# Kernel tuning notes

Hardware: AMD Instinct MI355X
Metric: run time of the kernel (lower is better)

The kernel has to match this reference:

```python
import jax, jax.numpy as jnp
import numpy as np

B = 64        # graphs per batch
NPG = 512     # nodes per graph (batch = repeat(arange(B), NPG))
D = 128       # hidden_dim = input_dim
L = 3         # GCN layers
K = 16        # NTN tensors
BINS = 16     # histogram bins


def _prep_edges(ei, N, dtype):
    # GCNConv normalization: add self-loops, deg on targets, sym norm
    loop = jnp.arange(N)
    src = jnp.concatenate([ei[0], loop])
    dst = jnp.concatenate([ei[1], loop])
    deg = jnp.zeros((N,), dtype).at[dst].add(1.0)
    dinv = jnp.where(deg > 0, jax.lax.rsqrt(deg), 0.0)
    norm = (dinv[src] * dinv[dst])[:, None]
    return src, dst, norm


def _encode(x, src, dst, norm, gcn_w, gcn_b, bn_g, bn_b, bn_m, bn_v):
    # eval-mode BatchNorm (running stats), dropout = identity
    for l in range(L):
        h = x @ gcn_w[l].T                     # [N, D]
        x = jnp.zeros_like(h).at[dst].add(norm * h[src]) + gcn_b[l]
        x = (x - bn_m[l]) * jax.lax.rsqrt(bn_v[l] + 1e-5) * bn_g[l] + bn_b[l]
        x = jax.nn.relu(x)
    return x


def _attention_pool(emb, ctx_w, ctx_b, att_w, att_b):
    t = jnp.tanh(emb @ ctx_w.T + ctx_b)        # [N, D]
    s = (t @ att_w + att_b).reshape(B, NPG, 1)
    e = emb.reshape(B, NPG, D)
    w = jax.nn.softmax(s, axis=1)              # per-graph softmax
    return (w * e).sum(axis=1)                 # [B, D]


def _histogram(e1, e2):
    n1 = (e1 / jnp.maximum(jnp.linalg.norm(e1, axis=-1, keepdims=True), 1e-8)).reshape(B, NPG, D)
    n2 = (e2 / jnp.maximum(jnp.linalg.norm(e2, axis=-1, keepdims=True), 1e-8)).reshape(B, NPG, D)
    sims = jnp.einsum('bnd,bmd->bnm', n1, n2)  # [B, n, n] cosine sims in [-1,1]
    bi = jnp.clip(jnp.floor((sims + 1.0) * (BINS / 2.0)), 0, BINS - 1).astype(jnp.int32)
    flat = (jnp.arange(B, dtype=jnp.int32)[:, None] * BINS + bi.reshape(B, -1)).reshape(-1)
    hist = jax.ops.segment_sum(jnp.ones(flat.shape, jnp.float32), flat,
                               num_segments=B * BINS).reshape(B, BINS)
    return hist / (hist.sum(axis=1, keepdims=True) + 1e-8)


def _ntn(g1, g2, T, tb, w1, b1, w2, b2, w3, b3):
    tp = jnp.einsum('bd,kde,be->bk', g1, T, g2) + tb   # bilinear products
    h = jax.nn.relu(tp @ w1.T + b1)
    h = jax.nn.relu(h @ w2.T + b2)
    return jax.nn.sigmoid(h @ w3.T + b3)               # [B, 1]


def _forward(x1, x2, edge_index1, edge_index2,
             gcn_w, gcn_b, bn_gamma, bn_beta, bn_mean, bn_var,
             ctx_w, ctx_b, att_w, att_b,
             ntn_T, ntn_bias, ntn_w1, ntn_b1, ntn_w2, ntn_b2, ntn_w3, ntn_b3,
             hist_w1, hist_b1, hist_w2, hist_b2,
             fus_w1, fus_b1, fus_w2, fus_b2):
    N = x1.shape[0]
    s1, d1, n1 = _prep_edges(edge_index1, N, x1.dtype)
    s2, d2, n2 = _prep_edges(edge_index2, N, x2.dtype)
    e1 = _encode(x1, s1, d1, n1, gcn_w, gcn_b, bn_gamma, bn_beta, bn_mean, bn_var)
    e2 = _encode(x2, s2, d2, n2, gcn_w, gcn_b, bn_gamma, bn_beta, bn_mean, bn_var)
    g1 = _attention_pool(e1, ctx_w, ctx_b, att_w, att_b)
    g2 = _attention_pool(e2, ctx_w, ctx_b, att_w, att_b)
    ntn_sim = _ntn(g1, g2, ntn_T, ntn_bias, ntn_w1, ntn_b1, ntn_w2, ntn_b2, ntn_w3, ntn_b3)
    hist = _histogram(e1, e2)
    hemb = jax.nn.relu(hist @ hist_w1.T + hist_b1) @ hist_w2.T + hist_b2
    comb = jnp.concatenate([ntn_sim, hemb], axis=1)    # [B, 17]
    h = jax.nn.relu(comb @ fus_w1.T + fus_b1)
    return jax.nn.sigmoid(h @ fus_w2.T + fus_b2)       # [B, 1]


def setup_inputs() -> dict:
    key = jax.random.key(0)
    ks = jax.random.split(key, 32)
    N = B * NPG
    E = 16 * N
    sc = 0.05
    inp = {
        'x1': jax.random.normal(ks[0], (N, D), jnp.float32),
        'x2': jax.random.normal(ks[1], (N, D), jnp.float32),
        'edge_index1': jax.random.randint(ks[2], (2, E), 0, N),
        'edge_index2': jax.random.randint(ks[3], (2, E), 0, N),
        'batch1': jnp.repeat(jnp.arange(B), NPG),
        'batch2': jnp.repeat(jnp.arange(B), NPG),
        'gcn_w': jax.random.normal(ks[4], (L, D, D), jnp.float32) * sc,
        'gcn_b': jax.random.normal(ks[5], (L, D), jnp.float32) * sc,
        'bn_gamma': jnp.ones((L, D), jnp.float32),
        'bn_beta': jnp.zeros((L, D), jnp.float32),
        'bn_mean': jnp.zeros((L, D), jnp.float32),
        'bn_var': jnp.ones((L, D), jnp.float32),
        'ctx_w': jax.random.normal(ks[6], (D, D), jnp.float32) * sc,
        'ctx_b': jax.random.normal(ks[7], (D,), jnp.float32) * sc,
        'att_w': jax.random.normal(ks[8], (D,), jnp.float32) * sc,
        'att_b': jax.random.normal(ks[9], (1,), jnp.float32) * sc,
        'ntn_T': jax.random.normal(ks[10], (K, D, D), jnp.float32) * 0.02,
        'ntn_bias': jax.random.normal(ks[11], (K,), jnp.float32) * sc,
        'ntn_w1': jax.random.normal(ks[12], (32, K), jnp.float32) * 0.2,
        'ntn_b1': jax.random.normal(ks[13], (32,), jnp.float32) * sc,
        'ntn_w2': jax.random.normal(ks[14], (16, 32), jnp.float32) * 0.15,
        'ntn_b2': jax.random.normal(ks[15], (16,), jnp.float32) * sc,
        'ntn_w3': jax.random.normal(ks[16], (1, 16), jnp.float32) * 0.2,
        'ntn_b3': jax.random.normal(ks[17], (1,), jnp.float32) * sc,
        'hist_w1': jax.random.normal(ks[18], (32, BINS), jnp.float32) * 0.2,
        'hist_b1': jax.random.normal(ks[19], (32,), jnp.float32) * sc,
        'hist_w2': jax.random.normal(ks[20], (16, 32), jnp.float32) * 0.15,
        'hist_b2': jax.random.normal(ks[21], (16,), jnp.float32) * sc,
        'fus_w1': jax.random.normal(ks[22], (8, 17), jnp.float32) * 0.2,
        'fus_b1': jax.random.normal(ks[23], (8,), jnp.float32) * sc,
        'fus_w2': jax.random.normal(ks[24], (1, 8), jnp.float32) * 0.3,
        'fus_b2': jax.random.normal(ks[25], (1,), jnp.float32) * sc,
    }
    return inp


def reference(x1, x2, edge_index1, edge_index2, batch1, batch2,
              gcn_w, gcn_b, bn_gamma, bn_beta, bn_mean, bn_var,
              ctx_w, ctx_b, att_w, att_b,
              ntn_T, ntn_bias, ntn_w1, ntn_b1, ntn_w2, ntn_b2, ntn_w3, ntn_b3,
              hist_w1, hist_b1, hist_w2, hist_b2,
              fus_w1, fus_b1, fus_w2, fus_b2):
    # batch1/batch2 encode 64 equal-sized graphs (repeat(arange(B), NPG));
    # the per-graph loops of the torch code become dense [B, NPG, D] ops.
    return _forward(x1, x2, edge_index1, edge_index2,
                    gcn_w, gcn_b, bn_gamma, bn_beta, bn_mean, bn_var,
                    ctx_w, ctx_b, att_w, att_b,
                    ntn_T, ntn_bias, ntn_w1, ntn_b1, ntn_w2, ntn_b2, ntn_w3, ntn_b3,
                    hist_w1, hist_b1, hist_w2, hist_b2,
                    fus_w1, fus_b1, fus_w2, fus_b2)
```

## Files before the change

kernel.cpp:

```cpp
#include <hip/hip_runtime.h>
#include <math.h>

#define NN 32768
#define BB 64
#define NPG 512
#define DD 128
#define LL 3
#define EE 524288
#define NBINS 16
#define KNTN 16
#define NND (NN*DD)
#define NBKT 128
#define BSEG 56
#define BCAPE 10240

typedef unsigned short ushort_t;
typedef __attribute__((ext_vector_type(8))) short short8;
typedef __attribute__((ext_vector_type(4))) float f32x4;

__device__ __forceinline__ ushort_t f2bf(float f) {
    unsigned u = __builtin_bit_cast(unsigned, f);
    u += 0x7FFFu + ((u >> 16) & 1u);
    return (ushort_t)(u >> 16);
}
__device__ __forceinline__ float bf2f(ushort_t h) {
    unsigned u = ((unsigned)h) << 16;
    return __builtin_bit_cast(float, u);
}
__device__ __forceinline__ unsigned pack2(float a, float b) {
    return (unsigned)f2bf(a) | ((unsigned)f2bf(b) << 16);
}
__device__ __forceinline__ float lo16(unsigned u) { return __builtin_bit_cast(float, u << 16); }
__device__ __forceinline__ float hi16(unsigned u) { return __builtin_bit_cast(float, u & 0xffff0000u); }

__global__ __launch_bounds__(256) void k_bucket(const int* __restrict__ ei1,
                                                const int* __restrict__ ei2,
                                                unsigned* __restrict__ ibuf,
                                                int* __restrict__ bcnt,
                                                const float* __restrict__ gw,
                                                const float* __restrict__ cw,
                                                ushort_t* __restrict__ wbf,
                                                const float* __restrict__ gcn_b,
                                                const float* __restrict__ bn_g,
                                                const float* __restrict__ bn_b,
                                                const float* __restrict__ bn_m,
                                                const float* __restrict__ bn_v,
                                                float* __restrict__ bnsc,
                                                float* __restrict__ bnsh) {
    int t = threadIdx.x;
    int blk = blockIdx.x;
    if (blk >= 512) {
        if (blk < 576) {
            int i = (blk - 512) * 256 + t;
            const float4 v = (i < 3 * DD * DD / 4) ? ((const float4*)gw)[i]
                                                   : ((const float4*)cw)[i - 3 * DD * DD / 4];
            uint2 o;
            o.x = pack2(v.x, v.y);
            o.y = pack2(v.z, v.w);
            ((uint2*)wbf)[i] = o;
        } else if (t < DD) {
            #pragma unroll
            for (int l = 0; l < LL; l++) {
                int c = l * DD + t;
                float sc = bn_g[c] * rsqrtf(bn_v[c] + 1e-5f);
                bnsc[c] = sc;
                bnsh[c] = (gcn_b[c] - bn_m[c]) * sc + bn_b[c];
            }
        }
        return;
    }
    __shared__ int cnt[NBKT];
    const int* ei = (blk < 256) ? ei1 : ei2;
    int ebase = (blk & 255) * 2048;
    int addn = (blk < 256) ? 0 : NN;
    for (int i = t; i < NBKT; i += 256) cnt[i] = 0;
    __syncthreads();
    #pragma unroll
    for (int k = 0; k < 8; k++) {
        int e = ebase + t + k * 256;
        int s = ei[e] + addn;
        int d = ei[EE + e] + addn;
        unsigned p = (unsigned)s | ((unsigned)d << 16);
        int bk = (unsigned)d >> 9;
        int rk = atomicAdd(&cnt[bk], 1);
        ibuf[(size_t)(bk * 512 + blk) * BSEG + rk] = p;
    }
    __syncthreads();
    if (t < NBKT) bcnt[t * 512 + blk] = cnt[t];
}

__global__ __launch_bounds__(256) void k_bcsr(const unsigned* __restrict__ ibuf,
                                              const int* __restrict__ bcnt,
                                              int* __restrict__ deg,
                                              float* __restrict__ dinv,
                                              int* __restrict__ rowstart,
                                              ushort_t* __restrict__ esrc) {
    __shared__ int cnt[512];
    __shared__ int ps[256];
    __shared__ int lcur[512];
    int bk = blockIdx.x, t = threadIdx.x;
    for (int i = t; i < 512; i += 256) cnt[i] = 0;
    __syncthreads();
    for (int b = t; b < 512; b += 256) {
        int n = bcnt[bk * 512 + b];
        const unsigned* seg = ibuf + (size_t)(bk * 512 + b) * BSEG;
        for (int i = 0; i < n; i++) {
            int dl = (seg[i] >> 16) & 511;
            atomicAdd(&cnt[dl], 1);
        }
    }
    __syncthreads();
    int c0 = cnt[2 * t], c1 = cnt[2 * t + 1];
    ps[t] = c0 + c1;
    __syncthreads();
    for (int o = 1; o < 256; o <<= 1) {
        int v = (t >= o) ? ps[t - o] : 0;
        __syncthreads();
        ps[t] += v;
        __syncthreads();
    }
    int excl = (t == 0) ? 0 : ps[t - 1];
    int base = bk * BCAPE;
    int g0 = bk * 512 + 2 * t, g1 = g0 + 1;
    deg[g0] = c0; deg[g1] = c1;
    dinv[g0] = rsqrtf((float)c0 + 1.0f);
    dinv[g1] = rsqrtf((float)c1 + 1.0f);
    int r0 = base + excl, r1 = base + excl + c0;
    rowstart[g0] = r0;
    rowstart[g1] = r1;
    lcur[2 * t] = r0;
    lcur[2 * t + 1] = r1;
    __syncthreads();
    for (int b = t; b < 512; b += 256) {
        int n = bcnt[bk * 512 + b];
        const unsigned* seg = ibuf + (size_t)(bk * 512 + b) * BSEG;
        for (int i = 0; i < n; i++) {
            unsigned p = seg[i];
            int dl = (p >> 16) & 511;
            int slot = atomicAdd(&lcur[dl], 1);
            esrc[slot] = (ushort_t)(p & 0xffffu);
        }
    }
}

template<int EPI, int XF>
__global__ __launch_bounds__(256) void k_mgemm(const ushort_t* __restrict__ X,
                                               const float* __restrict__ Xf1,
                                               const float* __restrict__ Xf2,
                                               const ushort_t* __restrict__ Wb,
                                               const float* __restrict__ bias,
                                               ushort_t* __restrict__ Out,
                                               const float* __restrict__ aw,
                                               const float* __restrict__ ab,
                                               float* __restrict__ Sout,
                                               const float* __restrict__ dscale) {
    __shared__ __align__(16) ushort_t wlds[128 * 128];
    int t = threadIdx.x;
    {
        int r = t >> 1, h = t & 1;
        const uint4* src = (const uint4*)(Wb + (size_t)r * DD + h * 64);
        #pragma unroll
        for (int i = 0; i < 8; i++) {
            int co = h * 128 + i * 16;
            int sw = co ^ ((r & 7) << 4);
            *(uint4*)&wlds[r * DD + (sw >> 1)] = src[i];
        }
    }
    __syncthreads();
    int w = t >> 6, l = t & 63;
    int rw = blockIdx.x * 128 + w * 32;
    int lr = l & 15, lg = l >> 4;
    f32x4 acc[2][8];
    #pragma unroll
    for (int g = 0; g < 2; g++)
        #pragma unroll
        for (int c = 0; c < 8; c++) acc[g][c] = (f32x4){0.f, 0.f, 0.f, 0.f};
    const ushort_t* xrow0 = X + (size_t)(rw + lr) * DD + lg * 8;
    const ushort_t* xrow1 = xrow0 + (size_t)16 * DD;
    const float* xf0 = nullptr;
    if (XF) {
        const float* xb = (rw < NN) ? Xf1 : (Xf2 - (size_t)NN * DD);
        xf0 = xb + (size_t)(rw + lr) * DD + lg * 8;
    }
    int swl = (lr & 7) << 4;
    for (int kt = 0; kt < 4; kt++) {
        short8 a0, a1;
        if (XF) {
            float4 va = *(const float4*)(xf0 + kt * 32);
            float4 vb = *(const float4*)(xf0 + kt * 32 + 4);
            float4 vc = *(const float4*)(xf0 + (size_t)16 * DD + kt * 32);
            float4 vd = *(const float4*)(xf0 + (size_t)16 * DD + kt * 32 + 4);
            a0[0] = (short)f2bf(va.x); a0[1] = (short)f2bf(va.y);
            a0[2] = (short)f2bf(va.z); a0[3] = (short)f2bf(va.w);
            a0[4] = (short)f2bf(vb.x); a0[5] = (short)f2bf(vb.y);
            a0[6] = (short)f2bf(vb.z); a0[7] = (short)f2bf(vb.w);
            a1[0] = (short)f2bf(vc.x); a1[1] = (short)f2bf(vc.y);
            a1[2] = (short)f2bf(vc.z); a1[3] = (short)f2bf(vc.w);
            a1[4] = (short)f2bf(vd.x); a1[5] = (short)f2bf(vd.y);
            a1[6] = (short)f2bf(vd.z); a1[7] = (short)f2bf(vd.w);
        } else {
            a0 = *(const short8*)(xrow0 + kt * 32);
            a1 = *(const short8*)(xrow1 + kt * 32);
        }
        int colsw = (kt * 64 + lg * 16) ^ swl;
        #pragma unroll
        for (int c = 0; c < 8; c++) {
            int row = c * 16 + lr;
            short8 b = *(const short8*)&wlds[row * DD + (colsw >> 1)];
            acc[0][c] = __builtin_amdgcn_mfma_f32_16x16x32_bf16(a0, b, acc[0][c], 0, 0, 0);
            acc[1][c] = __builtin_amdgcn_mfma_f32_16x16x32_bf16(a1, b, acc[1][c], 0, 0, 0);
        }
    }
    if (EPI == 0) {
        float ds[2][4];
        #pragma unroll
        for (int g = 0; g < 2; g++)
            #pragma unroll
            for (int q = 0; q < 4; q++) ds[g][q] = dscale[rw + g * 16 + lg * 4 + q];
        #pragma unroll
        for (int g = 0; g < 2; g++)
            #pragma unroll
            for (int c = 0; c < 8; c++) {
                int col = c * 16 + lr;
                #pragma unroll
                for (int q = 0; q < 4; q++)
                    Out[(size_t)(rw + g * 16 + lg * 4 + q) * DD + col] = f2bf(acc[g][c][q] * ds[g][q]);
            }
    } else {
        float rs[2][4] = {};
        #pragma unroll
        for (int c = 0; c < 8; c++) {
            int col = c * 16 + lr;
            float bv = bias[col], wv = aw[col];
            #pragma unroll
            for (int g = 0; g < 2; g++)
                #pragma unroll
                for (int q = 0; q < 4; q++)
                    rs[g][q] += tanhf(acc[g][c][q] + bv) * wv;
        }
        #pragma unroll
        for (int m = 1; m < 16; m <<= 1)
            #pragma unroll
            for (int g = 0; g < 2; g++)
                #pragma unroll
                for (int q = 0; q < 4; q++) rs[g][q] += __shfl_xor(rs[g][q], m);
        if (lr == 0) {
            float a0 = ab[0];
            #pragma unroll
            for (int g = 0; g < 2; g++)
                #pragma unroll
                for (int q = 0; q < 4; q++)
                    Sout[rw + g * 16 + lg * 4 + q] = rs[g][q] + a0;
        }
    }
}

#define GATHER(u, s) uint4 u = Hu4[(size_t)(s) * 16 + cl]
#define ACCUM(u) \
    a0 += lo16(u.x); a1 += hi16(u.x); a2 += lo16(u.y); a3 += hi16(u.y); \
    a4 += lo16(u.z); a5 += hi16(u.z); a6 += lo16(u.w); a7 += hi16(u.w)

template<int LAST>
__global__ __launch_bounds__(256) void k_agg(
    const ushort_t* __restrict__ Hs, const int* __restrict__ rowstart,
    const int* __restrict__ deg, const ushort_t* __restrict__ esrc,
    const float* __restrict__ dinv, const float* __restrict__ bnsc,
    const float* __restrict__ bnsh, ushort_t* __restrict__ A,
    ushort_t* __restrict__ Nrm) {
    __shared__ ushort_t sidx[2048];
    int nb0 = blockIdx.x * 16;
    int blockBeg = rowstart[nb0];
    int blockCnt = rowstart[nb0 + 15] + deg[nb0 + 15] - blockBeg;
    for (int i = threadIdx.x; i < blockCnt; i += 256) sidx[i] = esrc[blockBeg + i];
    __syncthreads();
    int l = threadIdx.x & 63;
    int q = l >> 4, cl = l & 15;
    int n = nb0 + (threadIdx.x >> 6) * 4 + q;
    const uint4* Hu4 = (const uint4*)Hs;
    int beg = rowstart[n] - blockBeg;
    int end = beg + deg[n];
    float di = dinv[n];
    uint4 h = Hu4[(size_t)n * 16 + cl];
    float a0 = lo16(h.x), a1 = hi16(h.x), a2 = lo16(h.y), a3 = hi16(h.y);
    float a4 = lo16(h.z), a5 = hi16(h.z), a6 = lo16(h.w), a7 = hi16(h.w);
    int j = beg;
    for (; j + 8 <= end; j += 8) {
        unsigned s0 = sidx[j + 0], s1 = sidx[j + 1], s2 = sidx[j + 2], s3 = sidx[j + 3];
        unsigned s4 = sidx[j + 4], s5 = sidx[j + 5], s6 = sidx[j + 6], s7 = sidx[j + 7];
        GATHER(u0, s0); GATHER(u1, s1); GATHER(u2, s2); GATHER(u3, s3);
        GATHER(u4, s4); GATHER(u5, s5); GATHER(u6, s6); GATHER(u7, s7);
        ACCUM(u0); ACCUM(u1); ACCUM(u2); ACCUM(u3);
        ACCUM(u4); ACCUM(u5); ACCUM(u6); ACCUM(u7);
    }
    for (; j + 2 <= end; j += 2) {
        unsigned s0 = sidx[j], s1 = sidx[j + 1];
        GATHER(u0, s0); GATHER(u1, s1);
        ACCUM(u0); ACCUM(u1);
    }
    if (j < end) {
        unsigned s0 = sidx[j];
        GATHER(u0, s0);
        ACCUM(u0);
    }
    int c = cl * 8;
    float4 scA = *(const float4*)&bnsc[c], scB = *(const float4*)&bnsc[c + 4];
    float4 shA = *(const float4*)&bnsh[c], shB = *(const float4*)&bnsh[c + 4];
    float o0 = fmaf(a0 * di, scA.x, shA.x);
    float o1 = fmaf(a1 * di, scA.y, shA.y);
    float o2 = fmaf(a2 * di, scA.z, shA.z);
    float o3 = fmaf(a3 * di, scA.w, shA.w);
    float o4 = fmaf(a4 * di, scB.x, shB.x);
    float o5 = fmaf(a5 * di, scB.y, shB.y);
    float o6 = fmaf(a6 * di, scB.z, shB.z);
    float o7 = fmaf(a7 * di, scB.w, shB.w);
    uint4 av;
    av.x = pack2(fmaxf(o0, 0.f), fmaxf(o1, 0.f));
    av.y = pack2(fmaxf(o2, 0.f), fmaxf(o3, 0.f));
    av.z = pack2(fmaxf(o4, 0.f), fmaxf(o5, 0.f));
    av.w = pack2(fmaxf(o6, 0.f), fmaxf(o7, 0.f));
    ((uint4*)A)[(size_t)n * 16 + cl] = av;
    if (LAST) {
        float r0 = lo16(av.x), r1 = hi16(av.x), r2 = lo16(av.y), r3 = hi16(av.y);
        float r4 = lo16(av.z), r5 = hi16(av.z), r6 = lo16(av.w), r7 = hi16(av.w);
        float ss = ((r0 * r0 + r1 * r1) + (r2 * r2 + r3 * r3)) +
                   ((r4 * r4 + r5 * r5) + (r6 * r6 + r7 * r7));
        #pragma unroll
        for (int o = 8; o > 0; o >>= 1) ss += __shfl_xor(ss, o);
        float inv = 1.0f / fmaxf(sqrtf(ss), 1e-8f);
        uint4 nv;
        nv.x = pack2(r0 * inv, r1 * inv);
        nv.y = pack2(r2 * inv, r3 * inv);
        nv.z = pack2(r4 * inv, r5 * inv);
        nv.w = pack2(r6 * inv, r7 * inv);
        ((uint4*)Nrm)[(size_t)n * 16 + cl] = nv;
    }
}

__global__ __launch_bounds__(512) void k_pool2(const float* __restrict__ S,
                                               const ushort_t* __restrict__ Emb,
                                               float* __restrict__ G) {
    int b = blockIdx.x, t = threadIdx.x;
    __shared__ float red[512];
    __shared__ float w[512];
    __shared__ float red0[512], red1[512];
    float s = S[b * NPG + t];
    red[t] = s;
    __syncthreads();
    for (int o = 256; o > 0; o >>= 1) { if (t < o) red[t] = fmaxf(red[t], red[t + o]); __syncthreads(); }
    float m = red[0];
    __syncthreads();
    float e = expf(s - m);
    w[t] = e;
    red[t] = e;
    __syncthreads();
    for (int o = 256; o > 0; o >>= 1) { if (t < o) red[t] += red[t + o]; __syncthreads(); }
    float inv = 1.0f / red[0];
    int l = t & 63, ch = t >> 6;
    int nbase = b * NPG + ch * 64;
    float a0 = 0.f, a1 = 0.f;
    #pragma unroll 4
    for (int i = 0; i < 64; i++) {
        float wv = w[ch * 64 + i];
        unsigned u = ((const unsigned*)(Emb + (size_t)(nbase + i) * DD))[l];
        a0 += wv * lo16(u);
        a1 += wv * hi16(u);
    }
    red0[t] = a0; red1[t] = a1;
    __syncthreads();
    if (t < 64) {
        float s0 = 0.f, s1 = 0.f;
        #pragma unroll
        for (int c = 0; c < 8; c++) { s0 += red0[t + c * 64]; s1 += red1[t + c * 64]; }
        G[b * DD + 2 * t] = s0 * inv;
        G[b * DD + 2 * t + 1] = s1 * inv;
    }
}

__global__ __launch_bounds__(256) void k_hist(const ushort_t* __restrict__ N1,
                                              const ushort_t* __restrict__ N2,
                                              float* __restrict__ Histp) {
    __shared__ __align__(16) ushort_t blds[128 * 128];
    __shared__ int hl[256 * 17];
    __shared__ float hred[NBINS];
    int t = threadIdx.x, w = t >> 6, l = t & 63;
    int lr = l & 15, lg = l >> 4;
    int g = blockIdx.x >> 4, ti = (blockIdx.x >> 2) & 3, tj = blockIdx.x & 3;
    {
        int r = t >> 1, h = t & 1;
        const uint4* src = (const uint4*)(N2 + ((size_t)g * NPG + tj * 128 + r) * DD + h * 64);
        #pragma unroll
        for (int i = 0; i < 8; i++) {
            int co = h * 128 + i * 16;
            int sw = co ^ ((r & 7) << 4);
            *(uint4*)&blds[r * DD + (sw >> 1)] = src[i];
        }
    }
    #pragma unroll
    for (int i = t; i < 256 * 17; i += 256) hl[i] = 0;
    if (t < NBINS) hred[t] = 0.f;
    __syncthreads();

    const ushort_t* arow = N1 + ((size_t)g * NPG + ti * 128 + w * 32 + lr) * DD + lg * 8;
    f32x4 acc[2][8];
    #pragma unroll
    for (int r = 0; r < 2; r++)
        #pragma unroll
        for (int c = 0; c < 8; c++) acc[r][c] = (f32x4){0.f, 0.f, 0.f, 0.f};
    int swl = (lr & 7) << 4;
    for (int kt = 0; kt < 4; kt++) {
        short8 a0 = *(const short8*)(arow + kt * 32);
        short8 a1 = *(const short8*)(arow + (size_t)16 * DD + kt * 32);
        int colsw = (kt * 64 + lg * 16) ^ swl;
        #pragma unroll
        for (int c = 0; c < 8; c++) {
            int row = c * 16 + lr;
            short8 b = *(const short8*)&blds[row * DD + (colsw >> 1)];
            acc[0][c] = __builtin_amdgcn_mfma_f32_16x16x32_bf16(a0, b, acc[0][c], 0, 0, 0);
            acc[1][c] = __builtin_amdgcn_mfma_f32_16x16x32_bf16(a1, b, acc[1][c], 0, 0, 0);
        }
    }
    int base = t * 17;
    #pragma unroll
    for (int r = 0; r < 2; r++)
        #pragma unroll
        for (int c = 0; c < 8; c++)
            #pragma unroll
            for (int q = 0; q < 4; q++) {
                float sim = acc[r][c][q];
                float v = floorf((sim + 1.0f) * 8.0f);
                v = fminf(fmaxf(v, 0.f), 15.f);
                atomicAdd(&hl[base + (int)v], 1);
            }
    __syncthreads();
    int bin = t & 15, r0 = (t >> 4) * 16;
    int s = 0;
    #pragma unroll
    for (int r = 0; r < 16; r++) s += hl[(r0 + r) * 17 + bin];
    atomicAdd(&hred[bin], (float)s);
    __syncthreads();
    if (t < NBINS) Histp[((size_t)g * 16 + (ti * 4 + tj)) * NBINS + t] = hred[t];
}

__global__ __launch_bounds__(128) void k_ntn(const float* __restrict__ G1,
                                             const float* __restrict__ G2,
                                             const float* __restrict__ T,
                                             const float* __restrict__ tb,
                                             float* __restrict__ TP) {
    int b = blockIdx.x, k = blockIdx.y;
    int e = threadIdx.x;
    const float* Tk = T + (size_t)k * DD * DD;
    float g2e = G2[b * DD + e];
    float acc = 0.f;
    for (int d = 0; d < DD; d++) acc += G1[b * DD + d] * Tk[(size_t)d * DD + e];
    float val = acc * g2e;
    #pragma unroll
    for (int o = 32; o > 0; o >>= 1) val += __shfl_down(val, o);
    __shared__ float ps[2];
    if ((e & 63) == 0) ps[e >> 6] = val;
    __syncthreads();
    if (e == 0) TP[b * KNTN + k] = ps[0] + ps[1] + tb[k];
}

__global__ __launch_bounds__(256) void k_final(const float* __restrict__ TP, const float* __restrict__ Histp,
                        const float* nw1, const float* nb1, const float* nw2, const float* nb2,
                        const float* nw3, const float* nb3,
                        const float* hw1, const float* hb1, const float* hw2, const float* hb2,
                        const float* fw1, const float* fb1, const float* fw2, const float* fb2,
                        float* __restrict__ out) {
    __shared__ float sTP[BB * 16], sHist[BB * 16];
    __shared__ float snw1[512], snw2[512], shw1[512], shw2[512];
    __shared__ float snw3[16], snb1[32], snb2[16], shb1[32], shb2[16];
    __shared__ float sfw1[136], sfb1[8], sfw2[8], sscal[2];
    int t = threadIdx.x;
    for (int i = t; i < BB * 16; i += 256) {
        sTP[i] = TP[i];
        int b = i >> 4, bin = i & 15;
        float s = 0.f;
        #pragma unroll
        for (int tile = 0; tile < 16; tile++) s += Histp[((size_t)b * 16 + tile) * NBINS + bin];
        sHist[i] = s;
    }
    for (int i = t; i < 512; i += 256) {
        snw1[i] = nw1[i]; snw2[i] = nw2[i]; shw1[i] = hw1[i]; shw2[i] = hw2[i];
    }
    if (t < 136) sfw1[t] = fw1[t];
    if (t < 32) { snb1[t] = nb1[t]; shb1[t] = hb1[t]; }
    if (t < 16) { snb2[t] = nb2[t]; shb2[t] = hb2[t]; snw3[t] = nw3[t]; }
    if (t < 8) { sfb1[t] = fb1[t]; sfw2[t] = fw2[t]; }
    if (t == 0) { sscal[0] = nb3[0]; sscal[1] = fb2[0]; }
    __syncthreads();
    if (t >= BB) return;
    int b = t;
    float h1[32];
    #pragma unroll
    for (int i = 0; i < 32; i++) {
        float a = snb1[i];
        for (int k = 0; k < 16; k++) a += sTP[b * 16 + k] * snw1[i * 16 + k];
        h1[i] = fmaxf(a, 0.f);
    }
    float h2[16];
    #pragma unroll
    for (int j = 0; j < 16; j++) {
        float a = snb2[j];
        for (int i = 0; i < 32; i++) a += h1[i] * snw2[j * 32 + i];
        h2[j] = fmaxf(a, 0.f);
    }
    float nt = sscal[0];
    for (int j = 0; j < 16; j++) nt += h2[j] * snw3[j];
    nt = 1.f / (1.f + expf(-nt));
    float hh[16]; float sum = 0.f;
    for (int k = 0; k < 16; k++) { hh[k] = sHist[b * 16 + k]; sum += hh[k]; }
    float inv = 1.f / (sum + 1e-8f);
    for (int k = 0; k < 16; k++) hh[k] *= inv;
    float g1v[32];
    #pragma unroll
    for (int i = 0; i < 32; i++) {
        float a = shb1[i];
        for (int k = 0; k < 16; k++) a += hh[k] * shw1[i * 16 + k];
        g1v[i] = fmaxf(a, 0.f);
    }
    float hemb[16];
    #pragma unroll
    for (int j = 0; j < 16; j++) {
        float a = shb2[j];
        for (int i = 0; i < 32; i++) a += g1v[i] * shw2[j * 32 + i];
        hemb[j] = a;
    }
    float comb[17];
    comb[0] = nt;
    for (int j = 0; j < 16; j++) comb[1 + j] = hemb[j];
    float f1[8];
    #pragma unroll
    for (int i = 0; i < 8; i++) {
        float a = sfb1[i];
        for (int j = 0; j < 17; j++) a += comb[j] * sfw1[i * 17 + j];
        f1[i] = fmaxf(a, 0.f);
    }
    float o = sscal[1];
    for (int i = 0; i < 8; i++) o += f1[i] * sfw2[i];
    out[b] = 1.f / (1.f + expf(-o));
}

extern "C" void kernel_launch(void* const* d_in, const int* in_sizes, int n_in,
                              void* d_out, int out_size, void* d_ws, size_t ws_size,
                              hipStream_t stream) {
    const float* x1    = (const float*)d_in[0];
    const float* x2    = (const float*)d_in[1];
    const int*   ei1   = (const int*)d_in[2];
    const int*   ei2   = (const int*)d_in[3];
    const float* gcn_w = (const float*)d_in[6];
    const float* gcn_b = (const float*)d_in[7];
    const float* bn_g  = (const float*)d_in[8];
    const float* bn_b  = (const float*)d_in[9];
    const float* bn_m  = (const float*)d_in[10];
    const float* bn_v  = (const float*)d_in[11];
    const float* ctx_w = (const float*)d_in[12];
    const float* ctx_b = (const float*)d_in[13];
    const float* att_w = (const float*)d_in[14];
    const float* att_b = (const float*)d_in[15];
    const float* ntn_T = (const float*)d_in[16];
    const float* ntn_b = (const float*)d_in[17];
    const float* nw1 = (const float*)d_in[18];
    const float* nb1 = (const float*)d_in[19];
    const float* nw2 = (const float*)d_in[20];
    const float* nb2 = (const float*)d_in[21];
    const float* nw3 = (const float*)d_in[22];
    const float* nb3 = (const float*)d_in[23];
    const float* hw1 = (const float*)d_in[24];
    const float* hb1 = (const float*)d_in[25];
    const float* hw2 = (const float*)d_in[26];
    const float* hb2 = (const float*)d_in[27];
    const float* fw1 = (const float*)d_in[28];
    const float* fb1 = (const float*)d_in[29];
    const float* fw2 = (const float*)d_in[30];
    const float* fb2 = (const float*)d_in[31];
    float* out = (float*)d_out;

    ushort_t* Xbf = (ushort_t*)d_ws;
    ushort_t* Abf = Xbf + 2 * (size_t)NND;
    ushort_t* Hbf = Abf + 2 * (size_t)NND;
    ushort_t* wbf = Hbf + 2 * (size_t)NND;
    float* dinv = (float*)(wbf + 4 * DD * DD);
    float* S    = dinv + 2 * NN;
    float* G    = S + 2 * NN;
    float* histp = G + 2 * BB * DD;
    float* tp   = histp + BB * 16 * NBINS;
    float* bnsc = tp + BB * KNTN;
    float* bnsh = bnsc + LL * DD;
    int* degi  = (int*)(bnsh + LL * DD);
    int* rowst = degi + 2 * NN;
    int* bcnt  = rowst + 2 * NN;
    ushort_t* esrc = (ushort_t*)(bcnt + NBKT * 512);
    unsigned* ibuf = (unsigned*)(esrc + (size_t)NBKT * BCAPE);

    k_bucket<<<577, 256, 0, stream>>>(ei1, ei2, ibuf, bcnt, gcn_w, ctx_w, wbf,
                                      gcn_b, bn_g, bn_b, bn_m, bn_v, bnsc, bnsh);
    k_bcsr<<<NBKT, 256, 0, stream>>>(ibuf, bcnt, degi, dinv, rowst, esrc);

    for (int l = 0; l < LL; l++) {
        if (l == 0)
            k_mgemm<0, 1><<<2 * NN / 128, 256, 0, stream>>>(nullptr, x1, x2,
                                                            wbf, nullptr, Hbf,
                                                            nullptr, nullptr, nullptr, dinv);
        else
            k_mgemm<0, 0><<<2 * NN / 128, 256, 0, stream>>>(Abf, nullptr, nullptr,
                                                            wbf + (size_t)l * DD * DD,
                                                            nullptr, Hbf, nullptr, nullptr, nullptr, dinv);
        if (l < LL - 1)
            k_agg<0><<<2 * NN / 16, 256, 0, stream>>>(Hbf, rowst, degi, esrc, dinv,
                                                      bnsc + l * DD, bnsh + l * DD, Abf, nullptr);
        else
            k_agg<1><<<2 * NN / 16, 256, 0, stream>>>(Hbf, rowst, degi, esrc, dinv,
                                                      bnsc + l * DD, bnsh + l * DD, Abf, Xbf);
    }
    k_mgemm<2, 0><<<2 * NN / 128, 256, 0, stream>>>(Abf, nullptr, nullptr,
                                                    wbf + 3 * DD * DD, ctx_b,
                                                    nullptr, att_w, att_b, S, nullptr);
    k_pool2<<<2 * BB, 512, 0, stream>>>(S, Abf, G);
    k_hist<<<BB * 16, 256, 0, stream>>>(Xbf, Xbf + NND, histp);
    k_ntn<<<dim3(BB, KNTN), 128, 0, stream>>>(G, G + BB * DD, ntn_T, ntn_b, tp);
    k_final<<<1, 256, 0, stream>>>(tp, histp, nw1, nb1, nw2, nb2, nw3, nb3,
                                   hw1, hb1, hw2, hb2, fw1, fb1, fw2, fb2, out);
}
```

Measured before the change: 216.3 us.

## Fuse aggregation with next-layer GEMM using aggregate-then-transform order

Layers 2 and 3 now aggregate the pre-scaled previous activations first, then run the 128x128 weight GEMM on the aggregated tile held in LDS, with BatchNorm, ReLU and the dinv pre-scale for the next layer applied in the epilogue. This uses linearity, (A·X)W = A·(XW), to drop one GEMM launch per layer and one round trip of the H buffer through global memory. The last layer also computes the row L2 normalisation from the MFMA accumulators. In exchange, blocks are larger (512 threads plus 32KB of LDS and a 3072-entry index cache), which may lower occupancy. Rounding also changes, since aggregation now runs on bf16 inputs before the GEMM, and the per-block edge count must fit in SCAP.

```diff
diff --git a/kernel.cpp b/kernel.cpp
--- a/kernel.cpp
+++ b/kernel.cpp
@@ -13,6 +13,7 @@
 #define NBKT 128
 #define BSEG 56
 #define BCAPE 10240
+#define SCAP 3072
 
 typedef unsigned short ushort_t;
 typedef __attribute__((ext_vector_type(8))) short short8;
@@ -260,13 +261,11 @@
     a0 += lo16(u.x); a1 += hi16(u.x); a2 += lo16(u.y); a3 += hi16(u.y); \
     a4 += lo16(u.z); a5 += hi16(u.z); a6 += lo16(u.w); a7 += hi16(u.w)
 
-template<int LAST>
-__global__ __launch_bounds__(256) void k_agg(
+__global__ __launch_bounds__(256) void k_agg0(
     const ushort_t* __restrict__ Hs, const int* __restrict__ rowstart,
     const int* __restrict__ deg, const ushort_t* __restrict__ esrc,
     const float* __restrict__ dinv, const float* __restrict__ bnsc,
-    const float* __restrict__ bnsh, ushort_t* __restrict__ A,
-    ushort_t* __restrict__ Nrm) {
+    const float* __restrict__ bnsh, ushort_t* __restrict__ As) {
     __shared__ ushort_t sidx[2048];
     int nb0 = blockIdx.x * 16;
     int blockBeg = rowstart[nb0];
@@ -314,25 +313,133 @@
     float o6 = fmaf(a6 * di, scB.z, shB.z);
     float o7 = fmaf(a7 * di, scB.w, shB.w);
     uint4 av;
-    av.x = pack2(fmaxf(o0, 0.f), fmaxf(o1, 0.f));
-    av.y = pack2(fmaxf(o2, 0.f), fmaxf(o3, 0.f));
-    av.z = pack2(fmaxf(o4, 0.f), fmaxf(o5, 0.f));
-    av.w = pack2(fmaxf(o6, 0.f), fmaxf(o7, 0.f));
-    ((uint4*)A)[(size_t)n * 16 + cl] = av;
-    if (LAST) {
-        float r0 = lo16(av.x), r1 = hi16(av.x), r2 = lo16(av.y), r3 = hi16(av.y);
-        float r4 = lo16(av.z), r5 = hi16(av.z), r6 = lo16(av.w), r7 = hi16(av.w);
-        float ss = ((r0 * r0 + r1 * r1) + (r2 * r2 + r3 * r3)) +
-                   ((r4 * r4 + r5 * r5) + (r6 * r6 + r7 * r7));
-        #pragma unroll
-        for (int o = 8; o > 0; o >>= 1) ss += __shfl_xor(ss, o);
-        float inv = 1.0f / fmaxf(sqrtf(ss), 1e-8f);
-        uint4 nv;
-        nv.x = pack2(r0 * inv, r1 * inv);
-        nv.y = pack2(r2 * inv, r3 * inv);
-        nv.z = pack2(r4 * inv, r5 * inv);
-        nv.w = pack2(r6 * inv, r7 * inv);
-        ((uint4*)Nrm)[(size_t)n * 16 + cl] = nv;
+    av.x = pack2(fmaxf(o0, 0.f) * di, fmaxf(o1, 0.f) * di);
+    av.y = pack2(fmaxf(o2, 0.f) * di, fmaxf(o3, 0.f) * di);
+    av.z = pack2(fmaxf(o4, 0.f) * di, fmaxf(o5, 0.f) * di);
+    av.w = pack2(fmaxf(o6, 0.f) * di, fmaxf(o7, 0.f) * di);
+    ((uint4*)As)[(size_t)n * 16 + cl] = av;
+}
+
+template<int LAST>
+__global__ __launch_bounds__(512) void k_fused(
+    const ushort_t* __restrict__ As, const int* __restrict__ rowstart,
+    const int* __restrict__ deg, const ushort_t* __restrict__ esrc,
+    const float* __restrict__ dinv, const ushort_t* __restrict__ Wb,
+    const float* __restrict__ bnsc, const float* __restrict__ bnsh,
+    ushort_t* __restrict__ Out, ushort_t* __restrict__ Nrm) {
+    __shared__ __align__(16) ushort_t zlds[128 * 128];
+    __shared__ ushort_t sidx[SCAP];
+    int t = threadIdx.x;
+    int nb0 = blockIdx.x * 128;
+    int blockBeg = rowstart[nb0];
+    int blockCnt = rowstart[nb0 + 127] + deg[nb0 + 127] - blockBeg;
+    for (int i = t; i < blockCnt; i += 512) sidx[i] = esrc[blockBeg + i];
+    __syncthreads();
+    {
+        int cl = t & 15, qd = t >> 4;
+        const uint4* Hu4 = (const uint4*)As;
+        #pragma unroll
+        for (int it = 0; it < 4; it++) {
+            int nloc = it * 32 + qd;
+            int n = nb0 + nloc;
+            int beg = rowstart[n] - blockBeg;
+            int end = beg + deg[n];
+            float di = dinv[n];
+            uint4 h = Hu4[(size_t)n * 16 + cl];
+            float a0 = lo16(h.x), a1 = hi16(h.x), a2 = lo16(h.y), a3 = hi16(h.y);
+            float a4 = lo16(h.z), a5 = hi16(h.z), a6 = lo16(h.w), a7 = hi16(h.w);
+            int j = beg;
+            for (; j + 8 <= end; j += 8) {
+                unsigned s0 = sidx[j + 0], s1 = sidx[j + 1], s2 = sidx[j + 2], s3 = sidx[j + 3];
+                unsigned s4 = sidx[j + 4], s5 = sidx[j + 5], s6 = sidx[j + 6], s7 = sidx[j + 7];
+                GATHER(u0, s0); GATHER(u1, s1); GATHER(u2, s2); GATHER(u3, s3);
+                GATHER(u4, s4); GATHER(u5, s5); GATHER(u6, s6); GATHER(u7, s7);
+                ACCUM(u0); ACCUM(u1); ACCUM(u2); ACCUM(u3);
+                ACCUM(u4); ACCUM(u5); ACCUM(u6); ACCUM(u7);
+            }
+            for (; j + 2 <= end; j += 2) {
+                unsigned s0 = sidx[j], s1 = sidx[j + 1];
+                GATHER(u0, s0); GATHER(u1, s1);
+                ACCUM(u0); ACCUM(u1);
+            }
+            if (j < end) {
+                unsigned s0 = sidx[j];
+                GATHER(u0, s0);
+                ACCUM(u0);
+            }
+            uint4 zv;
+            zv.x = pack2(a0 * di, a1 * di);
+            zv.y = pack2(a2 * di, a3 * di);
+            zv.z = pack2(a4 * di, a5 * di);
+            zv.w = pack2(a6 * di, a7 * di);
+            int bcol = (cl * 16) ^ ((nloc & 7) << 4);
+            *(uint4*)&zlds[nloc * DD + (bcol >> 1)] = zv;
+        }
+    }
+    __syncthreads();
+    int w = t >> 6, l = t & 63;
+    int lr = l & 15, lg = l >> 4;
+    int rl = w * 16 + lr;
+    f32x4 acc[8];
+    #pragma unroll
+    for (int c = 0; c < 8; c++) acc[c] = (f32x4){0.f, 0.f, 0.f, 0.f};
+    const ushort_t* wrow = Wb + (size_t)lr * DD + lg * 8;
+    int swl = (rl & 7) << 4;
+    for (int kt = 0; kt < 4; kt++) {
+        int bcol = (kt * 64 + lg * 16) ^ swl;
+        short8 a = *(const short8*)&zlds[rl * DD + (bcol >> 1)];
+        #pragma unroll
+        for (int c = 0; c < 8; c++) {
+            short8 b = *(const short8*)(wrow + (size_t)c * 16 * DD + kt * 32);
+            acc[c] = __builtin_amdgcn_mfma_f32_16x16x32_bf16(a, b, acc[c], 0, 0, 0);
+        }
+    }
+    int rowbase = nb0 + w * 16 + lg * 4;
+    if (!LAST) {
+        float ds[4];
+        #pragma unroll
+        for (int q = 0; q < 4; q++) ds[q] = dinv[rowbase + q];
+        #pragma unroll
+        for (int c = 0; c < 8; c++) {
+            int col = c * 16 + lr;
+            float sc = bnsc[col], sh = bnsh[col];
+            #pragma unroll
+            for (int q = 0; q < 4; q++) {
+                float v = fmaxf(fmaf(acc[c][q], sc, sh), 0.f);
+                Out[(size_t)(rowbase + q) * DD + col] = f2bf(v * ds[q]);
+            }
+        }
+    } else {
+        float sq[4] = {0.f, 0.f, 0.f, 0.f};
+        #pragma unroll
+        for (int c = 0; c < 8; c++) {
+            int col = c * 16 + lr;
+            float sc = bnsc[col], sh = bnsh[col];
+            #pragma unroll
+            for (int q = 0; q < 4; q++) {
+                float v = fmaxf(fmaf(acc[c][q], sc, sh), 0.f);
+                float r = bf2f(f2bf(v));
+                acc[c][q] = r;
+                sq[q] += r * r;
+            }
+        }
+        #pragma unroll
+        for (int m = 1; m < 16; m <<= 1)
+            #pragma unroll
+            for (int q = 0; q < 4; q++) sq[q] += __shfl_xor(sq[q], m);
+        float iv[4];
+        #pragma unroll
+        for (int q = 0; q < 4; q++) iv[q] = 1.0f / fmaxf(sqrtf(sq[q]), 1e-8f);
+        #pragma unroll
+        for (int c = 0; c < 8; c++) {
+            int col = c * 16 + lr;
+            #pragma unroll
+            for (int q = 0; q < 4; q++) {
+                float r = acc[c][q];
+                Out[(size_t)(rowbase + q) * DD + col] = f2bf(r);
+                Nrm[(size_t)(rowbase + q) * DD + col] = f2bf(r * iv[q]);
+            }
+        }
     }
 }
 
@@ -597,22 +704,17 @@
                                       gcn_b, bn_g, bn_b, bn_m, bn_v, bnsc, bnsh);
     k_bcsr<<<NBKT, 256, 0, stream>>>(ibuf, bcnt, degi, dinv, rowst, esrc);
 
-    for (int l = 0; l < LL; l++) {
-        if (l == 0)
-            k_mgemm<0, 1><<<2 * NN / 128, 256, 0, stream>>>(nullptr, x1, x2,
-                                                            wbf, nullptr, Hbf,
-                                                            nullptr, nullptr, nullptr, dinv);
-        else
-            k_mgemm<0, 0><<<2 * NN / 128, 256, 0, stream>>>(Abf, nullptr, nullptr,
-                                                            wbf + (size_t)l * DD * DD,
-                                                            nullptr, Hbf, nullptr, nullptr, nullptr, dinv);
-        if (l < LL - 1)
-            k_agg<0><<<2 * NN / 16, 256, 0, stream>>>(Hbf, rowst, degi, esrc, dinv,
-                                                      bnsc + l * DD, bnsh + l * DD, Abf, nullptr);
-        else
-            k_agg<1><<<2 * NN / 16, 256, 0, stream>>>(Hbf, rowst, degi, esrc, dinv,
-                                                      bnsc + l * DD, bnsh + l * DD, Abf, Xbf);
-    }
+    k_mgemm<0, 1><<<2 * NN / 128, 256, 0, stream>>>(nullptr, x1, x2, wbf, nullptr,
+                                                    Hbf, nullptr, nullptr, nullptr, dinv);
+    k_agg0<<<2 * NN / 16, 256, 0, stream>>>(Hbf, rowst, degi, esrc, dinv,
+                                            bnsc, bnsh, Abf);
+    k_fused<0><<<2 * NN / 128, 512, 0, stream>>>(Abf, rowst, degi, esrc, dinv,
+                                                 wbf + (size_t)1 * DD * DD,
+                                                 bnsc + 1 * DD, bnsh + 1 * DD, Hbf, nullptr);
+    k_fused<1><<<2 * NN / 128, 512, 0, stream>>>(Hbf, rowst, degi, esrc, dinv,
+                                                 wbf + (size_t)2 * DD * DD,
+                                                 bnsc + 2 * DD, bnsh + 2 * DD, Abf, Xbf);
+
     k_mgemm<2, 0><<<2 * NN / 128, 256, 0, stream>>>(Abf, nullptr, nullptr,
                                                     wbf + 3 * DD * DD, ctx_b,
                                                     nullptr, att_w, att_b, S, nullptr);
```

After: 229.9 us. 6.3% more time.
